# Performance work log

Measured on AMD Instinct MI355X. Metric: run time of the kernel, lower is better.

## Reference

```python
import math
import jax, jax.numpy as jnp
import numpy as np

QDEPTH = 8
WIDTH = 32
HEIGHT = 32
PIXELS = WIDTH * HEIGHT          # 1024
WIRES = int(math.ceil(math.log2(PIXELS)))  # 10, and PIXELS == 2**WIRES exactly
BATCH = 2048


def setup_inputs() -> dict:
    key = jax.random.key(0)
    k1, k2 = jax.random.split(key)
    x = jax.random.normal(k1, (BATCH, 1, WIDTH, HEIGHT), dtype=jnp.float32)
    # torch.randn(weight_shape) * 0.4
    weights = jax.random.normal(k2, (QDEPTH, WIRES, 3), dtype=jnp.float32) * 0.4
    return {"x": x, "weights": weights, "reps": 1}


def _apply_1q(s, U, wire):
    # s: (batch, 2, 2, ..., 2); apply 2x2 unitary U on qubit `wire` (axis wire+1)
    ax = wire + 1
    s = jnp.moveaxis(s, ax, -1)
    s = s @ U.T                      # new[..., i] = sum_j U[i, j] * old[..., j]
    return jnp.moveaxis(s, -1, ax)


def _apply_cnot(s, ctrl, tgt):
    # flip target bit on the control==1 half of the state
    c_ax = ctrl + 1
    t_ax = tgt + 1
    s0 = jnp.take(s, 0, axis=c_ax)
    s1 = jnp.take(s, 1, axis=c_ax)
    t = t_ax - 1 if t_ax > c_ax else t_ax
    s1 = jnp.flip(s1, axis=t)
    return jnp.stack([s0, s1], axis=c_ax)


def _rot_matrix(phi, theta, omega):
    # qml.Rot = RZ(phi) -> RY(theta) -> RZ(omega)
    c = jnp.cos(theta * 0.5)
    sn = jnp.sin(theta * 0.5)
    ep = jnp.exp(-0.5j * (phi + omega))   # e^{-i(phi+omega)/2}
    em = jnp.exp(-0.5j * (phi - omega))   # e^{-i(phi-omega)/2}
    return jnp.stack([
        jnp.stack([ep * c, -jnp.conj(em) * sn]),
        jnp.stack([em * sn, jnp.conj(ep) * c]),
    ]).astype(jnp.complex64)


def _circuit(psi, weights, reps):
    # psi: (batch, 2**WIRES) complex64 normalized state
    b = psi.shape[0]
    s = psi.reshape((b,) + (2,) * WIRES)
    w = jnp.tanh(weights)                 # qw_map.tanh
    # StronglyEntanglingLayers default ranges: r_l = l % (wires-1) + 1
    ranges = [(l % (WIRES - 1)) + 1 for l in range(QDEPTH)]
    for _ in range(reps):
        for l in range(QDEPTH):
            for q in range(WIRES):
                U = _rot_matrix(w[l, q, 0], w[l, q, 1], w[l, q, 2])
                s = _apply_1q(s, U, q)
            r = ranges[l]
            for q in range(WIRES):
                s = _apply_cnot(s, q, (q + r) % WIRES)
    return s.reshape(b, 2 ** WIRES)


def reference(x, weights, reps):
    b = x.shape[0]
    v = x.reshape(b, PIXELS)                       # b 1 w h -> b (w h)
    old_norm = jnp.linalg.norm(v, axis=-1, keepdims=True)
    psi = (v / old_norm).astype(jnp.complex64)     # real amplitudes, zero imag
    out = _circuit(psi, weights, reps)
    out = out * old_norm.astype(jnp.complex64)
    return out.reshape(b, 1, WIDTH, HEIGHT)
```

## Files before the change

### kernel.cpp

```cpp
#include <hip/hip_runtime.h>
#include <math.h>


#define WIRES   10
#define NSTATE  1024
#define QDEPTH  8
#define NBATCH  2048
#define NGATES  (QDEPTH * WIRES)

typedef float v2f __attribute__((ext_vector_type(2)));
typedef unsigned int v2u __attribute__((ext_vector_type(2)));
static __device__ __forceinline__ v2f s2(float x) { return (v2f){x, x}; }

__device__ __forceinline__ int perm_g(int j, int r) {
#pragma unroll
    for (int q = WIRES - 1; q >= 0; --q) {
        const int cb = 9 - q;
        const int tb = 9 - ((q + r) % WIRES);
        j ^= ((j >> cb) & 1) << tb;
    }
    return j;
}

#if __has_builtin(__builtin_amdgcn_readlane)
static __device__ __forceinline__ int rli(int v, int idx) {
    return __builtin_amdgcn_readlane(v, idx);
}
#else
static __device__ __forceinline__ int rli(int v, int idx) {
    return __shfl(v, idx, 64);
}
#endif
static __device__ __forceinline__ float rlf(float v, int idx) {
    return __int_as_float(rli(__float_as_int(v), idx));
}

template<int CTRL>
__device__ __forceinline__ float dppmov(float x) {
    return __int_as_float(__builtin_amdgcn_update_dpp(
        0, __float_as_int(x), CTRL, 0xF, 0xF, true));
}
#define FX1(v)  dppmov<0xB1>(v)
#define FX2(v)  dppmov<0x4E>(v)
#define FX4(v)  dppmov<0x1B>(dppmov<0x141>(v))
#define FX8(v)  dppmov<0x128>(v)

#if __has_builtin(__builtin_amdgcn_permlane16_swap)
static __device__ __forceinline__ float pl16swap(float x) {
    const v2u r = __builtin_amdgcn_permlane16_swap(
        __float_as_uint(x), __float_as_uint(x), false, false);
    return __uint_as_float((threadIdx.x & 16) ? r.x : r.y);
}
#define FX16(v) pl16swap(v)
#else
#define FX16(v) __shfl_xor((v), 16, 64)
#endif

#if __has_builtin(__builtin_amdgcn_permlane32_swap)
static __device__ __forceinline__ float pl32swap(float x) {
    const v2u r = __builtin_amdgcn_permlane32_swap(
        __float_as_uint(x), __float_as_uint(x), false, false);
    return __uint_as_float((threadIdx.x & 32) ? r.x : r.y);
}
#define FX32(v) pl32swap(v)
#else
#define FX32(v) __shfl_xor((v), 32, 64)
#endif

__device__ __forceinline__ void gate_coeffs(
    const float* __restrict__ w, int g, float (&c8)[8])
{
    const float phi   = tanhf(w[g * 3 + 0]);
    const float theta = tanhf(w[g * 3 + 1]);
    const float omega = tanhf(w[g * 3 + 2]);
    const float c  = cosf(theta * 0.5f);
    const float sn = sinf(theta * 0.5f);
    const float a  = 0.5f * (phi + omega);
    const float bb = 0.5f * (phi - omega);
    const float ca = cosf(a),  sa = sinf(a);
    const float cb = cosf(bb), sb = sinf(bb);
    c8[0] =  ca * c;  c8[1] = -sa * c;
    c8[2] = -cb * sn; c8[3] = -sb * sn;
    c8[4] =  cb * sn; c8[5] = -sb * sn;
    c8[6] =  ca * c;  c8[7] =  sa * c;
}

#define LOCAL_GATE(Q, MASK)                                                   \
    {                                                                         \
        const float u00r=getc(Q,0), u00i=getc(Q,1), u01r=getc(Q,2),           \
                    u01i=getc(Q,3), u10r=getc(Q,4), u10i=getc(Q,5),           \
                    u11r=getc(Q,6), u11i=getc(Q,7);                           \
        _Pragma("unroll")                                                     \
        for (int k0 = 0; k0 < 8; ++k0) {                                      \
            if (k0 & (MASK)) continue;                                        \
            const int k1 = k0 | (MASK);                                       \
            const v2f a0r = zr[k0], a0i = zi[k0];                             \
            const v2f a1r = zr[k1], a1i = zi[k1];                             \
            zr[k0] = s2(u00r)*a0r - s2(u00i)*a0i + s2(u01r)*a1r - s2(u01i)*a1i;\
            zi[k0] = s2(u00r)*a0i + s2(u00i)*a0r + s2(u01r)*a1i + s2(u01i)*a1r;\
            zr[k1] = s2(u10r)*a0r - s2(u10i)*a0i + s2(u11r)*a1r - s2(u11i)*a1i;\
            zi[k1] = s2(u10r)*a0i + s2(u10i)*a0r + s2(u11r)*a1i + s2(u11i)*a1r;\
        }                                                                     \
    }

#define HSWAP_GATE(Q)                                                         \
    {                                                                         \
        const float u00r=getc(Q,0), u00i=getc(Q,1), u01r=getc(Q,2),           \
                    u01i=getc(Q,3), u10r=getc(Q,4), u10i=getc(Q,5),           \
                    u11r=getc(Q,6), u11i=getc(Q,7);                           \
        const v2f pAr = (v2f){u00r, u11r};                                    \
        const v2f pAi = (v2f){u00i, u11i};                                    \
        const v2f pBr = (v2f){u01r, u10r};                                    \
        const v2f pBi = (v2f){u01i, u10i};                                    \
        _Pragma("unroll")                                                     \
        for (int k = 0; k < 8; ++k) {                                         \
            const v2f r  = zr[k], i = zi[k];                                  \
            const v2f rs = __builtin_shufflevector(r, r, 1, 0);               \
            const v2f is = __builtin_shufflevector(i, i, 1, 0);               \
            zr[k] = pAr*r - pAi*i + pBr*rs - pBi*is;                          \
            zi[k] = pAr*i + pAi*r + pBr*is + pBi*rs;                          \
        }                                                                     \
    }

#define LANE_GATE(Q, J, FETCH)                                                \
    {                                                                         \
        const float u00r=getc(Q,0), u00i=getc(Q,1), u01r=getc(Q,2),           \
                    u01i=getc(Q,3), u10r=getc(Q,4), u10i=getc(Q,5),           \
                    u11r=getc(Q,6), u11i=getc(Q,7);                           \
        const bool hi = (lane >> (J)) & 1;                                    \
        const float c0r = hi ? u11r : u00r, c0i = hi ? u11i : u00i;           \
        const float c1r = hi ? u10r : u01r, c1i = hi ? u10i : u01i;           \
        _Pragma("unroll")                                                     \
        for (int k = 0; k < 8; ++k) {                                         \
            v2f pr, pi;                                                       \
            pr.x = FETCH(zr[k].x); pr.y = FETCH(zr[k].y);                     \
            pi.x = FETCH(zi[k].x); pi.y = FETCH(zi[k].y);                     \
            const v2f sr = zr[k], si = zi[k];                                 \
            zr[k] = s2(c0r)*sr - s2(c0i)*si + s2(c1r)*pr - s2(c1i)*pi;        \
            zi[k] = s2(c0r)*si + s2(c0i)*sr + s2(c1r)*pi + s2(c1i)*pr;        \
        }                                                                     \
    }

template<typename GetC>
__device__ __forceinline__ void layer_body(
    v2f (&zr)[8], v2f (&zi)[8], GetC getc,
    const int G0, const int G1, const int G2, const int G3,
    const int ga, float* __restrict__ lds, const int lane)
{
    LOCAL_GATE(9, 1)
    LOCAL_GATE(8, 2)
    LOCAL_GATE(7, 4)
    HSWAP_GATE(6)
    LANE_GATE(5, 0, FX1)
    LANE_GATE(4, 1, FX2)
    LANE_GATE(3, 2, FX4)
    LANE_GATE(2, 3, FX8)
    LANE_GATE(1, 4, FX16)
    LANE_GATE(0, 5, FX32)

#pragma unroll
    for (int k = 0; k < 8; ++k) {
        const int w = k * 64 + lane;
        lds[w]        = zr[k].x;
        lds[w + 512]  = zr[k].y;
        lds[w + 1024] = zi[k].x;
        lds[w + 1536] = zi[k].y;
    }
    const int s01 = G0 ^ G1;
    const int gkt[8] = {0, G0, G1, s01, G2, G2 ^ G0, G2 ^ G1, G2 ^ s01};
#pragma unroll
    for (int k = 0; k < 8; ++k) {
        const int a0 = ga ^ gkt[k];
        const int a1 = a0 ^ G3;
        zr[k].x = lds[a0]; zi[k].x = lds[a0 + 1024];
        zr[k].y = lds[a1]; zi[k].y = lds[a1 + 1024];
    }
}

__global__ __launch_bounds__(64) void qsim_rl(
    const float* __restrict__ x,
    const float* __restrict__ weights,
    float* __restrict__ out,
    const int interleaved)
{
    __shared__ float lds[2 * NSTATE];
    __shared__ int   gaT[QDEPTH * 64];

    const int lane = threadIdx.x;
    const int b    = blockIdx.x;

    float cA[8], cB[8];
    gate_coeffs(weights, lane, cA);
    gate_coeffs(weights, 64 + (lane & 15), cB);

    int gv;
    {
        const int lg = (lane >> 2) & 7;
        const int bb = lane & 3;
        const int j  = perm_g(1 << bb, lg + 1);
        gv = ((j & 15) << 6) | (j >> 4);
    }
#pragma unroll
    for (int l = 0; l < QDEPTH; ++l) {
        const int j = perm_g(lane << 4, l + 1);
        gaT[l * 64 + lane] = ((j & 15) << 6) | (j >> 4);
    }

    v2f zr[8], zi[8];
    const float4* __restrict__ x4 =
        (const float4*)(x + ((size_t)b << 10) + (lane << 4));
    {
        const float4 v0 = x4[0], v1 = x4[1], v2 = x4[2], v3 = x4[3];
        zr[0].x=v0.x; zr[1].x=v0.y; zr[2].x=v0.z; zr[3].x=v0.w;
        zr[4].x=v1.x; zr[5].x=v1.y; zr[6].x=v1.z; zr[7].x=v1.w;
        zr[0].y=v2.x; zr[1].y=v2.y; zr[2].y=v2.z; zr[3].y=v2.w;
        zr[4].y=v3.x; zr[5].y=v3.y; zr[6].y=v3.z; zr[7].y=v3.w;
#pragma unroll
        for (int k = 0; k < 8; ++k) zi[k] = (v2f){0.f, 0.f};
    }

    int ga = gaT[lane];

#pragma unroll 1
    for (int l = 0; l < 6; ++l) {
        const int sb = l * 10;
        const int G0 = rli(gv, 4 * l + 0);
        const int G1 = rli(gv, 4 * l + 1);
        const int G2 = rli(gv, 4 * l + 2);
        const int G3 = rli(gv, 4 * l + 3);
        const int ga_nx = gaT[(l + 1) * 64 + lane];
        layer_body(zr, zi,
            [&](int q, int j) { return rlf(cA[j], sb + q); },
            G0, G1, G2, G3, ga, lds, lane);
        ga = ga_nx;
    }
    {
        const int G0 = rli(gv, 24), G1 = rli(gv, 25);
        const int G2 = rli(gv, 26), G3 = rli(gv, 27);
        const int ga_nx = gaT[7 * 64 + lane];
        layer_body(zr, zi,
            [&](int q, int j) {
                return (q < 4) ? rlf(cA[j], 60 + q) : rlf(cB[j], q - 4);
            },
            G0, G1, G2, G3, ga, lds, lane);
        ga = ga_nx;
    }
    {
        const int G0 = rli(gv, 28), G1 = rli(gv, 29);
        const int G2 = rli(gv, 30), G3 = rli(gv, 31);
        layer_body(zr, zi,
            [&](int q, int j) { return rlf(cB[j], 6 + q); },
            G0, G1, G2, G3, ga, lds, lane);
    }

    if (interleaved) {
        float2* __restrict__ o2 = (float2*)out;
        const size_t base = ((size_t)b << 10) + (lane << 4);
#pragma unroll
        for (int k = 0; k < 8; ++k) {
            o2[base + k]     = make_float2(zr[k].x, zi[k].x);
            o2[base + k + 8] = make_float2(zr[k].y, zi[k].y);
        }
    } else {
        float4* __restrict__ o4 = (float4*)(out + ((size_t)b << 10) + (lane << 4));
        o4[0] = make_float4(zr[0].x, zr[1].x, zr[2].x, zr[3].x);
        o4[1] = make_float4(zr[4].x, zr[5].x, zr[6].x, zr[7].x);
        o4[2] = make_float4(zr[0].y, zr[1].y, zr[2].y, zr[3].y);
        o4[3] = make_float4(zr[4].y, zr[5].y, zr[6].y, zr[7].y);
    }
}

extern "C" void kernel_launch(void* const* d_in, const int* in_sizes, int n_in,
                              void* d_out, int out_size, void* d_ws, size_t ws_size,
                              hipStream_t stream) {
    const float* x       = (const float*)d_in[0];
    const float* weights = (const float*)d_in[1];
    float* out = (float*)d_out;
    const int interleaved = (out_size >= 2 * NBATCH * NSTATE) ? 1 : 0;
    (void)d_ws; (void)ws_size;

    qsim_rl<<<NBATCH, 64, 0, stream>>>(x, weights, out, interleaved);
}
```

Baseline: 108.2 us.

## Exploit SU(2) gate structure to store four coefficients; stagger block start

Each Rot gate is SU(2), so u10 = -conj(u01) and u11 = conj(u00). The gate macros now keep only four coefficients per gate and rebuild the rest by sign flips, with the lane-dependent selection done by an XOR on the sign bit. This cuts per-lane coefficient registers and shuffles (getc). It also adds a per-block s_sleep delay based on block index, meant to stagger waves so they do not all contend for the same resources at once. The delay itself adds idle time.

```diff
diff --git a/kernel.cpp b/kernel.cpp
--- a/kernel.cpp
+++ b/kernel.cpp
@@ -67,8 +67,8 @@
 #define FX32(v) __shfl_xor((v), 32, 64)
 #endif
 
-__device__ __forceinline__ void gate_coeffs(
-    const float* __restrict__ w, int g, float (&c8)[8])
+__device__ __forceinline__ void gate_coeffs4(
+    const float* __restrict__ w, int g, float (&c4)[4])
 {
     const float phi   = tanhf(w[g * 3 + 0]);
     const float theta = tanhf(w[g * 3 + 1]);
@@ -79,17 +79,20 @@
     const float bb = 0.5f * (phi - omega);
     const float ca = cosf(a),  sa = sinf(a);
     const float cb = cosf(bb), sb = sinf(bb);
-    c8[0] =  ca * c;  c8[1] = -sa * c;
-    c8[2] = -cb * sn; c8[3] = -sb * sn;
-    c8[4] =  cb * sn; c8[5] = -sb * sn;
-    c8[6] =  ca * c;  c8[7] =  sa * c;
+    c4[0] =  ca * c;
+    c4[1] = -sa * c;
+    c4[2] = -cb * sn;
+    c4[3] = -sb * sn;
+}
+
+static __device__ __forceinline__ float sgnxor(float v, unsigned s) {
+    return __uint_as_float(__float_as_uint(v) ^ s);
 }
 
 #define LOCAL_GATE(Q, MASK)                                                   \
     {                                                                         \
-        const float u00r=getc(Q,0), u00i=getc(Q,1), u01r=getc(Q,2),           \
-                    u01i=getc(Q,3), u10r=getc(Q,4), u10i=getc(Q,5),           \
-                    u11r=getc(Q,6), u11i=getc(Q,7);                           \
+        const float u00r=getc(Q,0), u00i=getc(Q,1);                           \
+        const float u01r=getc(Q,2), u01i=getc(Q,3);                           \
         _Pragma("unroll")                                                     \
         for (int k0 = 0; k0 < 8; ++k0) {                                      \
             if (k0 & (MASK)) continue;                                        \
@@ -98,20 +101,19 @@
             const v2f a1r = zr[k1], a1i = zi[k1];                             \
             zr[k0] = s2(u00r)*a0r - s2(u00i)*a0i + s2(u01r)*a1r - s2(u01i)*a1i;\
             zi[k0] = s2(u00r)*a0i + s2(u00i)*a0r + s2(u01r)*a1i + s2(u01i)*a1r;\
-            zr[k1] = s2(u10r)*a0r - s2(u10i)*a0i + s2(u11r)*a1r - s2(u11i)*a1i;\
-            zi[k1] = s2(u10r)*a0i + s2(u10i)*a0r + s2(u11r)*a1i + s2(u11i)*a1r;\
+            zr[k1] = s2(u00r)*a1r + s2(u00i)*a1i - s2(u01r)*a0r - s2(u01i)*a0i;\
+            zi[k1] = s2(u00r)*a1i - s2(u00i)*a1r - s2(u01r)*a0i + s2(u01i)*a0r;\
         }                                                                     \
     }
 
 #define HSWAP_GATE(Q)                                                         \
     {                                                                         \
-        const float u00r=getc(Q,0), u00i=getc(Q,1), u01r=getc(Q,2),           \
-                    u01i=getc(Q,3), u10r=getc(Q,4), u10i=getc(Q,5),           \
-                    u11r=getc(Q,6), u11i=getc(Q,7);                           \
-        const v2f pAr = (v2f){u00r, u11r};                                    \
-        const v2f pAi = (v2f){u00i, u11i};                                    \
-        const v2f pBr = (v2f){u01r, u10r};                                    \
-        const v2f pBi = (v2f){u01i, u10i};                                    \
+        const float u00r=getc(Q,0), u00i=getc(Q,1);                           \
+        const float u01r=getc(Q,2), u01i=getc(Q,3);                           \
+        const v2f pAr = s2(u00r);                                             \
+        const v2f pAi = (v2f){u00i, -u00i};                                   \
+        const v2f pBr = (v2f){u01r, -u01r};                                   \
+        const v2f pBi = s2(u01i);                                             \
         _Pragma("unroll")                                                     \
         for (int k = 0; k < 8; ++k) {                                         \
             const v2f r  = zr[k], i = zi[k];                                  \
@@ -124,12 +126,11 @@
 
 #define LANE_GATE(Q, J, FETCH)                                                \
     {                                                                         \
-        const float u00r=getc(Q,0), u00i=getc(Q,1), u01r=getc(Q,2),           \
-                    u01i=getc(Q,3), u10r=getc(Q,4), u10i=getc(Q,5),           \
-                    u11r=getc(Q,6), u11i=getc(Q,7);                           \
-        const bool hi = (lane >> (J)) & 1;                                    \
-        const float c0r = hi ? u11r : u00r, c0i = hi ? u11i : u00i;           \
-        const float c1r = hi ? u10r : u01r, c1i = hi ? u10i : u01i;           \
+        const float u00r=getc(Q,0), u00i=getc(Q,1);                           \
+        const float u01r=getc(Q,2), u01i=getc(Q,3);                           \
+        const unsigned sgn = ((unsigned)(lane >> (J)) & 1u) << 31;            \
+        const float c0r = u00r,            c0i = sgnxor(u00i, sgn);           \
+        const float c1r = sgnxor(u01r, sgn), c1i = u01i;                      \
         _Pragma("unroll")                                                     \
         for (int k = 0; k < 8; ++k) {                                         \
             v2f pr, pi;                                                       \
@@ -177,7 +178,7 @@
     }
 }
 
-__global__ __launch_bounds__(64) void qsim_rl(
+__global__ __launch_bounds__(64) void qsim_rl2(
     const float* __restrict__ x,
     const float* __restrict__ weights,
     float* __restrict__ out,
@@ -189,9 +190,11 @@
     const int lane = threadIdx.x;
     const int b    = blockIdx.x;
 
-    float cA[8], cB[8];
-    gate_coeffs(weights, lane, cA);
-    gate_coeffs(weights, 64 + (lane & 15), cB);
+    for (int i = 0; i < (b & 7); ++i) __builtin_amdgcn_s_sleep(4);
+
+    float cA[4], cB[4];
+    gate_coeffs4(weights, lane, cA);
+    gate_coeffs4(weights, 64 + (lane & 15), cB);
 
     int gv;
     {
@@ -279,5 +282,5 @@
     const int interleaved = (out_size >= 2 * NBATCH * NSTATE) ? 1 : 0;
     (void)d_ws; (void)ws_size;
 
-    qsim_rl<<<NBATCH, 64, 0, stream>>>(x, weights, out, interleaved);
-}
+    qsim_rl2<<<NBATCH, 64, 0, stream>>>(x, weights, out, interleaved);
+}
```

After: 105.9 us (median of 2 runs). 2.2% less time.
